# Kernel optimization log

Hardware: AMD Instinct MI355X
Metric: run time of the kernel (lower is better)

## Reference

```python
import jax, jax.numpy as jnp
import numpy as np

B = 64        # batch
N = 1024      # num_nodes
D_IN = 2      # input feature dim per node
U = 64        # num_units (hidden)
K = 2         # max_diffusion_step


def setup_inputs() -> dict:
    key = jax.random.key(0)
    ks = jax.random.split(key, 8)
    inputs = jax.random.normal(ks[0], (B, N * D_IN), dtype=jnp.float32)
    hx = jax.random.normal(ks[1], (B, N * U), dtype=jnp.float32)
    # random-walk style supports: nonnegative, row-normalized -> stable Chebyshev recursion
    a0 = jax.random.uniform(ks[2], (N, N), dtype=jnp.float32)
    a1 = jax.random.uniform(ks[3], (N, N), dtype=jnp.float32)
    support0 = a0 / jnp.sum(a0, axis=1, keepdims=True)
    support1 = a1 / jnp.sum(a1, axis=1, keepdims=True)
    num_matrices = 2 * K + 1            # len(supports)*K + 1 = 5
    in_sz = (D_IN + U) * num_matrices   # 330
    # xavier-normal init
    std_o = float(np.sqrt(2.0 / (in_sz + 2 * U)))
    std_u = float(np.sqrt(2.0 / (in_sz + U)))
    weights_output = jax.random.normal(ks[4], (in_sz, 2 * U), dtype=jnp.float32) * std_o
    weights_update = jax.random.normal(ks[5], (in_sz, U), dtype=jnp.float32) * std_u
    biases_output = jnp.ones((2 * U,), dtype=jnp.float32)
    biases_update = jnp.zeros((U,), dtype=jnp.float32)
    return {"inputs": inputs, "hx": hx, "support0": support0, "support1": support1,
            "weights_output": weights_output, "biases_output": biases_output,
            "weights_update": weights_update, "biases_update": biases_update}


def _gconv(x_cat, supports, W, b, out_size):
    # x_cat: [B, N, F]  -> Chebyshev diffusion series then dense projection
    Bsz, Nn, F = x_cat.shape
    x0 = x_cat.transpose(1, 2, 0).reshape(Nn, F * Bsz)  # [N, F*B]
    xs = [x0]
    for S in supports:
        x1 = S @ x0
        xs.append(x1)
        xk1, xk2 = x1, x0
        for _ in range(2, K + 1):
            x2 = 2.0 * (S @ xk1) - xk2
            xs.append(x2)
            xk1, xk2 = x2, xk1
    M = len(xs)                                         # num_matrices
    x = jnp.stack(xs, axis=0)                           # [M, N, F*B]
    x = x.reshape(M, Nn, F, Bsz).transpose(3, 1, 2, 0)  # [B, N, F, M]
    x = x.reshape(Bsz * Nn, F * M)
    y = x @ W + b                                       # [B*N, out_size]
    return y.reshape(Bsz, Nn * out_size)


def reference(inputs, hx, support0, support1, weights_output, biases_output,
              weights_update, biases_update):
    supports = (support0, support1)
    xi = inputs.reshape(B, N, D_IN)
    hs = hx.reshape(B, N, U)
    cat = jnp.concatenate([xi, hs], axis=2)             # [B, N, D_IN+U]
    value = jax.nn.sigmoid(_gconv(cat, supports, weights_output, biases_output, 2 * U))
    value = value.reshape(B, N, 2 * U)
    r = value[..., :U].reshape(B, N * U)
    u = value[..., U:].reshape(B, N * U)
    cat2 = jnp.concatenate([xi, (r * hx).reshape(B, N, U)], axis=2)
    c = jnp.tanh(_gconv(cat2, supports, weights_update, biases_update, U))
    return u * hx + (1.0 - u) * c
```

## Files before the change

### kernel.cpp

```cpp
#include <hip/hip_runtime.h>


typedef unsigned short u16;
typedef unsigned int u32;
typedef short s16x8 __attribute__((ext_vector_type(8)));
typedef float f32x4 __attribute__((ext_vector_type(4)));
typedef u16 u16x4 __attribute__((ext_vector_type(4)));

#define NN 1024
#define NB 64
#define NF 66
#define NCOLS 4224
#define KPAD 352
#define ASTRIDE 360

__device__ __forceinline__ u16 f2bf(float f) {
  u32 u = __builtin_bit_cast(u32, f);
  u = (u + 0x7fffu + ((u >> 16) & 1u)) >> 16;
  return (u16)u;
}
__device__ __forceinline__ float bf2f(u16 h) {
  u32 u = ((u32)h) << 16;
  return __builtin_bit_cast(float, u);
}

__device__ __forceinline__ void gload16(const void* g, void* l) {
  __builtin_amdgcn_global_load_lds(
      (const __attribute__((address_space(1))) u32*)g,
      (__attribute__((address_space(3))) u32*)l, 16, 0, 0);
}

#define CHEB_WAIT(N)                                      \
  do {                                                    \
    asm volatile("s_waitcnt vmcnt(" #N ")" ::: "memory"); \
    __builtin_amdgcn_s_barrier();                         \
    asm volatile("" ::: "memory");                        \
  } while (0)


__global__ __launch_bounds__(256) void pack_supports(
    const float* __restrict__ s0, const float* __restrict__ s1,
    u16* __restrict__ Acat, u16* __restrict__ ST0, u16* __restrict__ ST1) {
  __shared__ float tile[64][65];
  const int z = blockIdx.y;
  const float* S = z ? s1 : s0;
  u16* ST = z ? ST1 : ST0;
  const int r0 = (blockIdx.x >> 4) * 64, c0 = (blockIdx.x & 15) * 64;
  const int t = threadIdx.x;
  const size_t sbase = (size_t)z * 2048 * NN;
  int cc4 = (t & 15) * 4, rr = t >> 4;
#pragma unroll
  for (int p = 0; p < 4; p++) {
    int r = p * 16 + rr;
    f32x4 v = *(const f32x4*)(S + (size_t)(r0 + r) * NN + c0 + cc4);
    tile[r][cc4] = v.x; tile[r][cc4 + 1] = v.y;
    tile[r][cc4 + 2] = v.z; tile[r][cc4 + 3] = v.w;
    u16x4 o;
    o.x = f2bf(v.x); o.y = f2bf(v.y); o.z = f2bf(v.z); o.w = f2bf(v.w);
    *(u16x4*)&Acat[sbase + (size_t)(r0 + r) * NN + c0 + cc4] = o;
  }
  __syncthreads();
  int rr4 = (t & 15) * 4, cc = t >> 4;
#pragma unroll
  for (int p = 0; p < 4; p++) {
    int c = p * 16 + cc;
    u16x4 o;
    o.x = f2bf(tile[rr4][c]);     o.y = f2bf(tile[rr4 + 1][c]);
    o.z = f2bf(tile[rr4 + 2][c]); o.w = f2bf(tile[rr4 + 3][c]);
    *(u16x4*)&ST[(size_t)(c0 + c) * NN + r0 + rr4] = o;
  }
}

__global__ __launch_bounds__(64) void pack_w(
    const float* __restrict__ W, u16* __restrict__ Wt, int ldo) {
  int o = blockIdx.y;
  int kp = blockIdx.x * 64 + threadIdx.x;
  if (kp >= KPAD) return;
  float v = 0.f;
  if (kp < 330) {
    int m = kp / 66;
    int f = kp - m * 66;
    v = W[(f * 5 + m) * ldo + o];
  }
  Wt[(size_t)o * KPAD + kp] = f2bf(v);
}

__global__ __launch_bounds__(256) void pack_x0_inputs(
    const float* __restrict__ inp, u16* __restrict__ x0t, u16* __restrict__ x0pt) {
  int b = blockIdx.x, t = threadIdx.x;
  int n4 = t * 4;
  const float* src = inp + b * 2048 + n4 * 2;
  f32x4 a = *(const f32x4*)src;
  f32x4 c = *(const f32x4*)(src + 4);
  u16x4 r0, r1;
  r0.x = f2bf(a.x); r0.y = f2bf(a.z); r0.z = f2bf(c.x); r0.w = f2bf(c.z);
  r1.x = f2bf(a.y); r1.y = f2bf(a.w); r1.z = f2bf(c.y); r1.w = f2bf(c.w);
  size_t o0 = (size_t)(b)*NN + n4;
  size_t o1 = (size_t)(64 + b) * NN + n4;
  *(u16x4*)(x0t + o0) = r0;  *(u16x4*)(x0t + o1) = r1;
  *(u16x4*)(x0pt + o0) = r0; *(u16x4*)(x0pt + o1) = r1;
}

__global__ __launch_bounds__(256) void pack_x0_hx(
    const float* __restrict__ hx, u16* __restrict__ x0t) {
  __shared__ float tile[64][65];
  int n0 = blockIdx.x * 64, b = blockIdx.y, t = threadIdx.x;
  int u4 = (t & 15) * 4, r0 = t >> 4;
#pragma unroll
  for (int p = 0; p < 4; p++) {
    int row = p * 16 + r0;
    f32x4 v = *(const f32x4*)(hx + ((size_t)b << 16) + (size_t)(n0 + row) * 64 + u4);
    tile[row][u4] = v.x; tile[row][u4 + 1] = v.y;
    tile[row][u4 + 2] = v.z; tile[row][u4 + 3] = v.w;
  }
  __syncthreads();
  int n4 = (t & 15) * 4, uu0 = t >> 4;
#pragma unroll
  for (int p = 0; p < 4; p++) {
    int u = p * 16 + uu0;
    u16x4 o;
    o.x = f2bf(tile[n4][u]);     o.y = f2bf(tile[n4 + 1][u]);
    o.z = f2bf(tile[n4 + 2][u]); o.w = f2bf(tile[n4 + 3][u]);
    *(u16x4*)&x0t[(size_t)((2 + u) * 64 + b) * NN + n0 + n4] = o;
  }
}


__device__ __forceinline__ void gemm128_pipe(
    const u16* pAr, const u16* pBr,
    u16* As, u16* Bs,
    int w, int lane, f32x4 acc[4][4]) {
  const int db0 = (w * 32) * 32;
  const int db1 = (w * 32 + 16) * 32;
  const u16* pA0 = pAr; const u16* pA1 = pAr + (size_t)16 * NN;
  const u16* pB0 = pBr; const u16* pB1 = pBr + (size_t)16 * NN;
  const int wm = (w >> 1) * 64;
  const int wn = (w & 1) * 64;
  const int fr = lane & 15;
  const int q = lane >> 4;
  const int fo = (q ^ ((fr >> 1) & 3)) * 8;

  auto stage = [&](int buf) {
    u16* dA = As + buf * (128 * 32);
    u16* dB = Bs + buf * (128 * 32);
    gload16(pA0, dA + db0);
    gload16(pA1, dA + db1);
    gload16(pB0, dB + db0);
    gload16(pB1, dB + db1);
    pA0 += 32; pA1 += 32; pB0 += 32; pB1 += 32;
  };
  auto compute = [&](int buf) {
    const u16* cA = As + buf * (128 * 32);
    const u16* cB = Bs + buf * (128 * 32);
    s16x8 af[4], bfr[4];
#pragma unroll
    for (int i = 0; i < 4; i++)
      af[i] = *(const s16x8*)&cA[(wm + i * 16 + fr) * 32 + fo];
#pragma unroll
    for (int j = 0; j < 4; j++)
      bfr[j] = *(const s16x8*)&cB[(wn + j * 16 + fr) * 32 + fo];
#pragma unroll
    for (int i = 0; i < 4; i++)
#pragma unroll
      for (int j = 0; j < 4; j++)
        acc[i][j] = __builtin_amdgcn_mfma_f32_16x16x32_bf16(af[i], bfr[j], acc[i][j], 0, 0, 0);
  };

  stage(0); stage(1); stage(2);
#pragma unroll 1
  for (int it = 0; it < 7; it++) {
    CHEB_WAIT(8); stage(3); compute(0);
    CHEB_WAIT(8); stage(0); compute(1);
    CHEB_WAIT(8); stage(1); compute(2);
    CHEB_WAIT(8); stage(2); compute(3);
  }
  CHEB_WAIT(8); stage(3); compute(0);
  CHEB_WAIT(8); compute(1);
  CHEB_WAIT(4); compute(2);
  CHEB_WAIT(0); compute(3);
}

__global__ __launch_bounds__(256, 2) void gconv_gemm(
    const u16* __restrict__ Acat, const u16* __restrict__ Bx,
    u16* __restrict__ X1, u16* __restrict__ X2,
    u16* __restrict__ X3, u16* __restrict__ X4) {
  __shared__ u16 As[4][128 * 32];
  __shared__ u16 Bs[4][128 * 32];
  const int t = threadIdx.x;
  const int lane = t & 63;
  const int w = t >> 6;

  const int lid = blockIdx.x;
  const int work = (lid & 7) * 132 + (lid >> 3);
  const int mt = work / 33;
  const int nt = work % 33;

  const int rl = lane >> 2;
  const int swz = ((lane & 3) ^ ((lane >> 3) & 3)) * 8;
  const u16* pAr = Acat + (size_t)(mt * 128 + w * 32 + rl) * NN + swz;
  const u16* pBr = Bx + (size_t)(nt * 128 + w * 32 + rl) * NN + swz;

  f32x4 acc[4][4];
#pragma unroll
  for (int i = 0; i < 4; i++)
#pragma unroll
    for (int j = 0; j < 4; j++) acc[i][j] = f32x4{0.f, 0.f, 0.f, 0.f};

  gemm128_pipe(pAr, pBr, &As[0][0], &Bs[0][0], w, lane, acc);

  const int md = mt >> 3;
  u16* Xo = md == 0 ? X1 : md == 1 ? X2 : md == 2 ? X3 : X4;
  const int m0 = (mt & 7) * 128;
  const int n0 = nt * 128;
  const int wm = (w >> 1) * 64;
  const int wn = (w & 1) * 64;
  const int fr = lane & 15;
  const int nr0 = (lane >> 4) << 2;
#pragma unroll
  for (int i = 0; i < 4; i++) {
    const int node = m0 + wm + i * 16 + nr0;
#pragma unroll
    for (int j = 0; j < 4; j++) {
      const int colg = n0 + wn + j * 16 + fr;
      f32x4 c = acc[i][j];
      u16x4 o;
      o.x = f2bf(c.x); o.y = f2bf(c.y); o.z = f2bf(c.z); o.w = f2bf(c.w);
      *(u16x4*)&Xo[(size_t)colg * NN + node] = o;
    }
  }
}

__global__ __launch_bounds__(256, 2) void sq_gemm(
    const u16* __restrict__ ST0, const u16* __restrict__ ST1, u16* Acat) {
  __shared__ u16 As[4][128 * 32];
  __shared__ u16 Bs[4][128 * 32];
  const int t = threadIdx.x;
  const int lane = t & 63;
  const int w = t >> 6;

  const int lid = blockIdx.x;
  const int work = (lid & 7) * 16 + (lid >> 3);
  const int z = work >> 6;
  const int rr = work & 63;
  const int mtile = rr >> 3, ntile = rr & 7;

  const u16* A = z ? ST1 : ST0;
  const u16* B = Acat + (size_t)(z * 2048) * NN;

  const int rl = lane >> 2;
  const int swz = ((lane & 3) ^ ((lane >> 3) & 3)) * 8;
  const u16* pAr = A + (size_t)(mtile * 128 + w * 32 + rl) * NN + swz;
  const u16* pBr = B + (size_t)(ntile * 128 + w * 32 + rl) * NN + swz;

  f32x4 acc[4][4];
#pragma unroll
  for (int i = 0; i < 4; i++)
#pragma unroll
    for (int j = 0; j < 4; j++) acc[i][j] = f32x4{0.f, 0.f, 0.f, 0.f};

  gemm128_pipe(pAr, pBr, &As[0][0], &Bs[0][0], w, lane, acc);

  const size_t tbase = z ? 3072 : 1024;
  const int wm = (w >> 1) * 64;
  const int wn = (w & 1) * 64;
  const int fr = lane & 15;
  const int nr0 = (lane >> 4) << 2;
#pragma unroll
  for (int i = 0; i < 4; i++) {
    const int node = mtile * 128 + wm + i * 16 + nr0;
#pragma unroll
    for (int j = 0; j < 4; j++) {
      const int colg = ntile * 128 + wn + j * 16 + fr;
      f32x4 c = acc[i][j];
      u16x4 o;
      o.x = f2bf(2.f * c.x - (float)(node + 0 == colg));
      o.y = f2bf(2.f * c.y - (float)(node + 1 == colg));
      o.z = f2bf(2.f * c.z - (float)(node + 2 == colg));
      o.w = f2bf(2.f * c.w - (float)(node + 3 == colg));
      *(u16x4*)&Acat[(tbase + (size_t)colg) * NN + node] = o;
    }
  }
}


__device__ __forceinline__ void proj_stage(
    u16* A, const u16* __restrict__ X0, const u16* __restrict__ X1,
    const u16* __restrict__ X2, const u16* __restrict__ X3,
    const u16* __restrict__ X4, int b, int n0, int t) {
  for (int idx = t; idx < 1408; idx += 256) {
    const int kp0 = (idx >> 4) * 4;
    const int n4 = (idx & 15) * 4;
    u16x4 v[4];
#pragma unroll
    for (int r = 0; r < 4; r++) {
      const int kp = kp0 + r;
      if (kp < 330) {
        const int m = kp / 66;
        const int f = kp - m * 66;
        const u16* Xm = m == 0 ? X0 : m == 1 ? X1 : m == 2 ? X2 : m == 3 ? X3 : X4;
        v[r] = *(const u16x4*)(Xm + (size_t)(f * 64 + b) * NN + n0 + n4);
      } else {
        v[r] = u16x4{0, 0, 0, 0};
      }
    }
#pragma unroll
    for (int c = 0; c < 4; c++) {
      u16x4 o;
      o.x = v[0][c]; o.y = v[1][c]; o.z = v[2][c]; o.w = v[3][c];
      *(u16x4*)&A[(n4 + c) * ASTRIDE + kp0] = o;
    }
  }
}

__global__ __launch_bounds__(256) void proj1(
    const u16* __restrict__ X0, const u16* __restrict__ X1, const u16* __restrict__ X2,
    const u16* __restrict__ X3, const u16* __restrict__ X4,
    const u16* __restrict__ Wt, const float* __restrict__ bias,
    const float* __restrict__ hx, u16* __restrict__ X0p, float* __restrict__ uout) {
  __shared__ u16 A[64 * ASTRIDE];
  const int t = threadIdx.x;
  const int n0 = blockIdx.x * 64;
  const int b = blockIdx.y;
  proj_stage(A, X0, X1, X2, X3, X4, b, n0, t);
  __syncthreads();

  const int lane = t & 63;
  const int w = t >> 6;
  const int fr = lane & 15;
  const int q8 = (lane >> 4) * 8;
  const u16* arow = &A[(w * 16 + fr) * ASTRIDE + q8];

  f32x4 acc[8];
#pragma unroll
  for (int j = 0; j < 8; j++) acc[j] = f32x4{0.f, 0.f, 0.f, 0.f};

  for (int kc = 0; kc < KPAD; kc += 32) {
    const s16x8 af = *(const s16x8*)(arow + kc);
#pragma unroll
    for (int j = 0; j < 8; j++) {
      const s16x8 bf = *(const s16x8*)&Wt[(size_t)(j * 16 + fr) * KPAD + kc + q8];
      acc[j] = __builtin_amdgcn_mfma_f32_16x16x32_bf16(af, bf, acc[j], 0, 0, 0);
    }
  }

  const int nl0 = (lane >> 4) * 4;
  const int n = n0 + w * 16 + nl0;
#pragma unroll
  for (int j = 0; j < 8; j++) {
    const int o = j * 16 + fr;
    const float bs = bias[o];
    f32x4 v;
    v.x = 1.f / (1.f + __expf(-(acc[j].x + bs)));
    v.y = 1.f / (1.f + __expf(-(acc[j].y + bs)));
    v.z = 1.f / (1.f + __expf(-(acc[j].z + bs)));
    v.w = 1.f / (1.f + __expf(-(acc[j].w + bs)));
    if (o < 64) {
      const float* hxp = hx + ((size_t)b << 16) + (size_t)n * 64 + o;
      u16x4 s;
      s.x = f2bf(v.x * hxp[0 * 64]);
      s.y = f2bf(v.y * hxp[1 * 64]);
      s.z = f2bf(v.z * hxp[2 * 64]);
      s.w = f2bf(v.w * hxp[3 * 64]);
      *(u16x4*)&X0p[(size_t)((2 + o) * 64 + b) * NN + n] = s;
    } else {
      float* up = uout + (((size_t)b << 10) + n) * 64 + (o - 64);
      up[0 * 64] = v.x; up[1 * 64] = v.y; up[2 * 64] = v.z; up[3 * 64] = v.w;
    }
  }
}

__global__ __launch_bounds__(256) void proj2(
    const u16* __restrict__ X0, const u16* __restrict__ X1, const u16* __restrict__ X2,
    const u16* __restrict__ X3, const u16* __restrict__ X4,
    const u16* __restrict__ Wt, const float* __restrict__ bias,
    const float* __restrict__ hx, const float* uin, float* out) {
  __shared__ u16 A[64 * ASTRIDE];
  const int t = threadIdx.x;
  const int n0 = blockIdx.x * 64;
  const int b = blockIdx.y;
  proj_stage(A, X0, X1, X2, X3, X4, b, n0, t);
  __syncthreads();

  const int lane = t & 63;
  const int w = t >> 6;
  const int fr = lane & 15;
  const int q8 = (lane >> 4) * 8;
  const u16* arow = &A[(w * 16 + fr) * ASTRIDE + q8];

  f32x4 acc[4];
#pragma unroll
  for (int j = 0; j < 4; j++) acc[j] = f32x4{0.f, 0.f, 0.f, 0.f};

  for (int kc = 0; kc < KPAD; kc += 32) {
    const s16x8 af = *(const s16x8*)(arow + kc);
#pragma unroll
    for (int j = 0; j < 4; j++) {
      const s16x8 bf = *(const s16x8*)&Wt[(size_t)(j * 16 + fr) * KPAD + kc + q8];
      acc[j] = __builtin_amdgcn_mfma_f32_16x16x32_bf16(af, bf, acc[j], 0, 0, 0);
    }
  }

  const int nl0 = (lane >> 4) * 4;
  const int n = n0 + w * 16 + nl0;
#pragma unroll
  for (int j = 0; j < 4; j++) {
    const int o = j * 16 + fr;
    const float bs = bias[o];
    const size_t base = (((size_t)b << 10) + n) * 64 + o;
    float c0 = tanhf(acc[j].x + bs);
    float c1 = tanhf(acc[j].y + bs);
    float c2 = tanhf(acc[j].z + bs);
    float c3 = tanhf(acc[j].w + bs);
    float u0 = uin[base + 0 * 64], u1 = uin[base + 1 * 64];
    float u2 = uin[base + 2 * 64], u3 = uin[base + 3 * 64];
    float h0 = hx[base + 0 * 64], h1 = hx[base + 1 * 64];
    float h2 = hx[base + 2 * 64], h3 = hx[base + 3 * 64];
    out[base + 0 * 64] = u0 * h0 + (1.f - u0) * c0;
    out[base + 1 * 64] = u1 * h1 + (1.f - u1) * c1;
    out[base + 2 * 64] = u2 * h2 + (1.f - u2) * c2;
    out[base + 3 * 64] = u3 * h3 + (1.f - u3) * c3;
  }
}


extern "C" void kernel_launch(void* const* d_in, const int* in_sizes, int n_in,
                              void* d_out, int out_size, void* d_ws, size_t ws_size,
                              hipStream_t stream) {
  (void)in_sizes; (void)n_in; (void)out_size; (void)ws_size;
  const float* inp = (const float*)d_in[0];
  const float* hx  = (const float*)d_in[1];
  const float* s0  = (const float*)d_in[2];
  const float* s1  = (const float*)d_in[3];
  const float* Wo  = (const float*)d_in[4];
  const float* bo  = (const float*)d_in[5];
  const float* Wu  = (const float*)d_in[6];
  const float* bu  = (const float*)d_in[7];
  float* out = (float*)d_out;

  char* p = (char*)d_ws;
  u16* Acat = (u16*)p; p += (size_t)4096 * NN * 2;
  u16* ST0  = (u16*)p; p += (size_t)NN * NN * 2;
  u16* ST1  = (u16*)p; p += (size_t)NN * NN * 2;
  const size_t xbytes = (size_t)NCOLS * NN * 2;
  u16* X0T = (u16*)p; p += xbytes;
  u16* X1T = (u16*)p; p += xbytes;
  u16* X2T = (u16*)p; p += xbytes;
  u16* X3T = (u16*)p; p += xbytes;
  u16* X4T = (u16*)p; p += xbytes;
  u16* X0P = (u16*)p; p += xbytes;
  u16* Wt1 = (u16*)p; p += (size_t)128 * KPAD * 2;
  u16* Wt2 = (u16*)p; p += (size_t)64 * KPAD * 2;

  pack_supports<<<dim3(256, 2), dim3(256), 0, stream>>>(s0, s1, Acat, ST0, ST1);
  sq_gemm<<<dim3(128), dim3(256), 0, stream>>>(ST0, ST1, Acat);
  pack_w<<<dim3(6, 128), dim3(64), 0, stream>>>(Wo, Wt1, 128);
  pack_w<<<dim3(6, 64), dim3(64), 0, stream>>>(Wu, Wt2, 64);
  pack_x0_inputs<<<dim3(64), dim3(256), 0, stream>>>(inp, X0T, X0P);
  pack_x0_hx<<<dim3(16, 64), dim3(256), 0, stream>>>(hx, X0T);
  gconv_gemm<<<dim3(1056), dim3(256), 0, stream>>>(Acat, X0T, X1T, X2T, X3T, X4T);
  proj1<<<dim3(16, 64), dim3(256), 0, stream>>>(X0T, X1T, X2T, X3T, X4T, Wt1, bo, hx, X0P, out);
  gconv_gemm<<<dim3(1056), dim3(256), 0, stream>>>(Acat, X0P, X1T, X2T, X3T, X4T);
  proj2<<<dim3(16, 64), dim3(256), 0, stream>>>(X0P, X1T, X2T, X3T, X4T, Wt2, bu, hx, out, out);
}
```

Baseline: 320.4 us.

## Enlarge GEMM tiles to 256x128 with triple-buffered LDS pipeline

Changes the shared GEMM from 128x128 to 256x128 tiles. Each wave now computes a 128x64 sub-tile with 8x4 MFMA accumulators, and the LDS pipeline drops from four to three stages. The goal is more arithmetic per byte loaded and fewer blocks (528 for gconv, 64 for sq_gemm), at the cost of doubling accumulator registers, which may lower occupancy or cause spills. sq_gemm's 64 blocks underfill the GPU, which risks worse utilization there.

```diff
diff --git a/kernel.cpp b/kernel.cpp
--- a/kernel.cpp
+++ b/kernel.cpp
@@ -126,98 +126,96 @@
 }
 
 
-__device__ __forceinline__ void gemm128_pipe(
-    const u16* pAr, const u16* pBr,
+__device__ __forceinline__ void gemm256_pipe(
+    const u16* pA, const u16* pB,
     u16* As, u16* Bs,
-    int w, int lane, f32x4 acc[4][4]) {
-  const int db0 = (w * 32) * 32;
-  const int db1 = (w * 32 + 16) * 32;
-  const u16* pA0 = pAr; const u16* pA1 = pAr + (size_t)16 * NN;
-  const u16* pB0 = pBr; const u16* pB1 = pBr + (size_t)16 * NN;
-  const int wm = (w >> 1) * 64;
+    int w, int lane, f32x4 acc[8][4]) {
+  const int dbA = (w * 64) * 32;
+  const int dbB = (w * 32) * 32;
+  const u16* a0 = pA;
+  const u16* b0 = pB;
+  const int wm = (w >> 1) * 128;
   const int wn = (w & 1) * 64;
   const int fr = lane & 15;
   const int q = lane >> 4;
   const int fo = (q ^ ((fr >> 1) & 3)) * 8;
 
   auto stage = [&](int buf) {
-    u16* dA = As + buf * (128 * 32);
+    u16* dA = As + buf * (256 * 32);
     u16* dB = Bs + buf * (128 * 32);
-    gload16(pA0, dA + db0);
-    gload16(pA1, dA + db1);
-    gload16(pB0, dB + db0);
-    gload16(pB1, dB + db1);
-    pA0 += 32; pA1 += 32; pB0 += 32; pB1 += 32;
+    gload16(a0, dA + dbA);
+    gload16(a0 + (size_t)16 * NN, dA + dbA + 16 * 32);
+    gload16(a0 + (size_t)32 * NN, dA + dbA + 32 * 32);
+    gload16(a0 + (size_t)48 * NN, dA + dbA + 48 * 32);
+    gload16(b0, dB + dbB);
+    gload16(b0 + (size_t)16 * NN, dB + dbB + 16 * 32);
+    a0 += 32; b0 += 32;
   };
   auto compute = [&](int buf) {
-    const u16* cA = As + buf * (128 * 32);
+    const u16* cA = As + buf * (256 * 32);
     const u16* cB = Bs + buf * (128 * 32);
-    s16x8 af[4], bfr[4];
-#pragma unroll
-    for (int i = 0; i < 4; i++)
-      af[i] = *(const s16x8*)&cA[(wm + i * 16 + fr) * 32 + fo];
+    s16x8 bfr[4];
 #pragma unroll
     for (int j = 0; j < 4; j++)
       bfr[j] = *(const s16x8*)&cB[(wn + j * 16 + fr) * 32 + fo];
 #pragma unroll
-    for (int i = 0; i < 4; i++)
+    for (int i = 0; i < 8; i++) {
+      const s16x8 af = *(const s16x8*)&cA[(wm + i * 16 + fr) * 32 + fo];
 #pragma unroll
       for (int j = 0; j < 4; j++)
-        acc[i][j] = __builtin_amdgcn_mfma_f32_16x16x32_bf16(af[i], bfr[j], acc[i][j], 0, 0, 0);
+        acc[i][j] = __builtin_amdgcn_mfma_f32_16x16x32_bf16(af, bfr[j], acc[i][j], 0, 0, 0);
+    }
   };
 
-  stage(0); stage(1); stage(2);
+  stage(0); stage(1);
 #pragma unroll 1
-  for (int it = 0; it < 7; it++) {
-    CHEB_WAIT(8); stage(3); compute(0);
-    CHEB_WAIT(8); stage(0); compute(1);
-    CHEB_WAIT(8); stage(1); compute(2);
-    CHEB_WAIT(8); stage(2); compute(3);
-  }
-  CHEB_WAIT(8); stage(3); compute(0);
-  CHEB_WAIT(8); compute(1);
-  CHEB_WAIT(4); compute(2);
-  CHEB_WAIT(0); compute(3);
+  for (int it = 0; it < 10; it++) {
+    CHEB_WAIT(6); stage(2); compute(0);
+    CHEB_WAIT(6); stage(0); compute(1);
+    CHEB_WAIT(6); stage(1); compute(2);
+  }
+  CHEB_WAIT(6); compute(0);
+  CHEB_WAIT(0); compute(1);
 }
 
 __global__ __launch_bounds__(256, 2) void gconv_gemm(
     const u16* __restrict__ Acat, const u16* __restrict__ Bx,
     u16* __restrict__ X1, u16* __restrict__ X2,
     u16* __restrict__ X3, u16* __restrict__ X4) {
-  __shared__ u16 As[4][128 * 32];
-  __shared__ u16 Bs[4][128 * 32];
+  __shared__ u16 As[3][256 * 32];
+  __shared__ u16 Bs[3][128 * 32];
   const int t = threadIdx.x;
   const int lane = t & 63;
   const int w = t >> 6;
 
   const int lid = blockIdx.x;
-  const int work = (lid & 7) * 132 + (lid >> 3);
+  const int work = (lid & 7) * 66 + (lid >> 3);
   const int mt = work / 33;
   const int nt = work % 33;
 
   const int rl = lane >> 2;
   const int swz = ((lane & 3) ^ ((lane >> 3) & 3)) * 8;
-  const u16* pAr = Acat + (size_t)(mt * 128 + w * 32 + rl) * NN + swz;
-  const u16* pBr = Bx + (size_t)(nt * 128 + w * 32 + rl) * NN + swz;
-
-  f32x4 acc[4][4];
-#pragma unroll
-  for (int i = 0; i < 4; i++)
+  const u16* pA = Acat + (size_t)(mt * 256 + w * 64 + rl) * NN + swz;
+  const u16* pB = Bx + (size_t)(nt * 128 + w * 32 + rl) * NN + swz;
+
+  f32x4 acc[8][4];
+#pragma unroll
+  for (int i = 0; i < 8; i++)
 #pragma unroll
     for (int j = 0; j < 4; j++) acc[i][j] = f32x4{0.f, 0.f, 0.f, 0.f};
 
-  gemm128_pipe(pAr, pBr, &As[0][0], &Bs[0][0], w, lane, acc);
-
-  const int md = mt >> 3;
+  gemm256_pipe(pA, pB, &As[0][0], &Bs[0][0], w, lane, acc);
+
+  const int md = mt >> 2;
   u16* Xo = md == 0 ? X1 : md == 1 ? X2 : md == 2 ? X3 : X4;
-  const int m0 = (mt & 7) * 128;
+  const int m0 = (mt & 3) * 256;
   const int n0 = nt * 128;
-  const int wm = (w >> 1) * 64;
+  const int wm = (w >> 1) * 128;
   const int wn = (w & 1) * 64;
   const int fr = lane & 15;
   const int nr0 = (lane >> 4) << 2;
 #pragma unroll
-  for (int i = 0; i < 4; i++) {
+  for (int i = 0; i < 8; i++) {
     const int node = m0 + wm + i * 16 + nr0;
 #pragma unroll
     for (int j = 0; j < 4; j++) {
@@ -232,16 +230,15 @@
 
 __global__ __launch_bounds__(256, 2) void sq_gemm(
     const u16* __restrict__ ST0, const u16* __restrict__ ST1, u16* Acat) {
-  __shared__ u16 As[4][128 * 32];
-  __shared__ u16 Bs[4][128 * 32];
+  __shared__ u16 As[3][256 * 32];
+  __shared__ u16 Bs[3][128 * 32];
   const int t = threadIdx.x;
   const int lane = t & 63;
   const int w = t >> 6;
 
   const int lid = blockIdx.x;
-  const int work = (lid & 7) * 16 + (lid >> 3);
-  const int z = work >> 6;
-  const int rr = work & 63;
+  const int z = lid >> 5;
+  const int rr = lid & 31;
   const int mtile = rr >> 3, ntile = rr & 7;
 
   const u16* A = z ? ST1 : ST0;
@@ -249,25 +246,25 @@
 
   const int rl = lane >> 2;
   const int swz = ((lane & 3) ^ ((lane >> 3) & 3)) * 8;
-  const u16* pAr = A + (size_t)(mtile * 128 + w * 32 + rl) * NN + swz;
-  const u16* pBr = B + (size_t)(ntile * 128 + w * 32 + rl) * NN + swz;
-
-  f32x4 acc[4][4];
-#pragma unroll
-  for (int i = 0; i < 4; i++)
+  const u16* pA = A + (size_t)(mtile * 256 + w * 64 + rl) * NN + swz;
+  const u16* pB = B + (size_t)(ntile * 128 + w * 32 + rl) * NN + swz;
+
+  f32x4 acc[8][4];
+#pragma unroll
+  for (int i = 0; i < 8; i++)
 #pragma unroll
     for (int j = 0; j < 4; j++) acc[i][j] = f32x4{0.f, 0.f, 0.f, 0.f};
 
-  gemm128_pipe(pAr, pBr, &As[0][0], &Bs[0][0], w, lane, acc);
+  gemm256_pipe(pA, pB, &As[0][0], &Bs[0][0], w, lane, acc);
 
   const size_t tbase = z ? 3072 : 1024;
-  const int wm = (w >> 1) * 64;
+  const int wm = (w >> 1) * 128;
   const int wn = (w & 1) * 64;
   const int fr = lane & 15;
   const int nr0 = (lane >> 4) << 2;
 #pragma unroll
-  for (int i = 0; i < 4; i++) {
-    const int node = mtile * 128 + wm + i * 16 + nr0;
+  for (int i = 0; i < 8; i++) {
+    const int node = mtile * 256 + wm + i * 16 + nr0;
 #pragma unroll
     for (int j = 0; j < 4; j++) {
       const int colg = ntile * 128 + wn + j * 16 + fr;
@@ -452,13 +449,13 @@
   u16* Wt2 = (u16*)p; p += (size_t)64 * KPAD * 2;
 
   pack_supports<<<dim3(256, 2), dim3(256), 0, stream>>>(s0, s1, Acat, ST0, ST1);
-  sq_gemm<<<dim3(128), dim3(256), 0, stream>>>(ST0, ST1, Acat);
+  sq_gemm<<<dim3(64), dim3(256), 0, stream>>>(ST0, ST1, Acat);
   pack_w<<<dim3(6, 128), dim3(64), 0, stream>>>(Wo, Wt1, 128);
   pack_w<<<dim3(6, 64), dim3(64), 0, stream>>>(Wu, Wt2, 64);
   pack_x0_inputs<<<dim3(64), dim3(256), 0, stream>>>(inp, X0T, X0P);
   pack_x0_hx<<<dim3(16, 64), dim3(256), 0, stream>>>(hx, X0T);
-  gconv_gemm<<<dim3(1056), dim3(256), 0, stream>>>(Acat, X0T, X1T, X2T, X3T, X4T);
+  gconv_gemm<<<dim3(528), dim3(256), 0, stream>>>(Acat, X0T, X1T, X2T, X3T, X4T);
   proj1<<<dim3(16, 64), dim3(256), 0, stream>>>(X0T, X1T, X2T, X3T, X4T, Wt1, bo, hx, X0P, out);
-  gconv_gemm<<<dim3(1056), dim3(256), 0, stream>>>(Acat, X0P, X1T, X2T, X3T, X4T);
+  gconv_gemm<<<dim3(528), dim3(256), 0, stream>>>(Acat, X0P, X1T, X2T, X3T, X4T);
   proj2<<<dim3(16, 64), dim3(256), 0, stream>>>(X0P, X1T, X2T, X3T, X4T, Wt2, bu, hx, out, out);
 }
```

New measurement: 338.9 us. 5.8% more time.
